# Kernel tuning notes

Hardware: AMD Instinct MI355X
Metric: run time of the kernel (lower is better)

The kernel has to match this reference:

```python
import jax, jax.numpy as jnp
import numpy as np

ALPHA = 0.2   # LeakyReLU negative slope
NEG_INF = -9e15

def setup_inputs() -> dict:
    key = jax.random.key(0)
    k1, k2, k3, k4, k5 = jax.random.split(key, 5)
    B, N, F_IN, F_OUT = 8, 2048, 128, 128
    input = jax.random.normal(k1, (B, N, F_IN), dtype=jnp.float32)
    adj = jax.random.randint(k2, (B, N, N), 0, 2, dtype=jnp.int32)
    W = jax.random.normal(k3, (F_OUT, F_IN), dtype=jnp.float32) * (1.0 / np.sqrt(F_IN))
    a_src = jax.random.normal(k4, (F_OUT, 1), dtype=jnp.float32) * 0.1
    a_dst = jax.random.normal(k5, (F_OUT, 1), dtype=jnp.float32) * 0.1
    return {"input": input, "adj": adj, "W": W, "a_src": a_src, "a_dst": a_dst}

def reference(input, adj, W, a_src, a_dst):
    # h = input @ W^T : [B,N,F_out]
    h = jnp.einsum('bnf,of->bno', input, W)
    src = h @ a_src              # [B,N,1]
    dst = h @ a_dst              # [B,N,1]
    e = src + jnp.swapaxes(dst, 1, 2)          # [B,N,N] additive scores
    e = jnp.where(e > 0, e, ALPHA * e)         # LeakyReLU
    att = jnp.where(adj > 0, e, NEG_INF)
    att = jax.nn.softmax(att, axis=2)
    # dropout is identity in eval mode
    h_prime = jnp.einsum('bnm,bmo->bno', att, h)
    return jax.nn.elu(h_prime)                 # concat=True path
```

## Files before the change

### kernel.cpp

```cpp
#include <hip/hip_runtime.h>
#include <stdint.h>

#define NB 8
#define NN 2048
#define FF 128
#define ALPHA 0.2f

typedef unsigned short u16;
typedef __attribute__((ext_vector_type(8))) short bf16x8;
typedef __attribute__((ext_vector_type(4))) float f32x4;

__device__ __forceinline__ float bf2f(u16 h) {
    union { uint32_t u; float f; } v; v.u = ((uint32_t)h) << 16; return v.f;
}
__device__ __forceinline__ u16 f2bf(float x) {
    union { float f; uint32_t u; } v; v.f = x;
    uint32_t r = v.u + 0x7fffu + ((v.u >> 16) & 1u);
    return (u16)(r >> 16);
}
__device__ __forceinline__ uint4 pack8(const float o[8]) {
    uint4 r;
    r.x = (uint32_t)f2bf(o[0]) | ((uint32_t)f2bf(o[1]) << 16);
    r.y = (uint32_t)f2bf(o[2]) | ((uint32_t)f2bf(o[3]) << 16);
    r.z = (uint32_t)f2bf(o[4]) | ((uint32_t)f2bf(o[5]) << 16);
    r.w = (uint32_t)f2bf(o[6]) | ((uint32_t)f2bf(o[7]) << 16);
    return r;
}
__device__ __forceinline__ void load8f(const float* p, size_t i, float o[8]) {
    float4 a = *(const float4*)(p + i);
    float4 b = *(const float4*)(p + i + 4);
    o[0]=a.x; o[1]=a.y; o[2]=a.z; o[3]=a.w;
    o[4]=b.x; o[5]=b.y; o[6]=b.z; o[7]=b.w;
}

__device__ __forceinline__ void gload_lds16(const void* g, void* l) {
    __builtin_amdgcn_global_load_lds(
        (const __attribute__((address_space(1))) void*)g,
        (__attribute__((address_space(3))) void*)l,
        16, 0, 0);
}

__global__ __launch_bounds__(256) void k_prep(
    const float* __restrict__ x,
    const float* __restrict__ w,
    const float* __restrict__ as_,
    const float* __restrict__ ad_,
    u16* __restrict__ hT,
    float* __restrict__ srcp, float* __restrict__ dstp)
{
    __shared__ __attribute__((aligned(16))) u16 Ws[128][136];
    __shared__ __attribute__((aligned(16))) u16 Xs[64][136];
    __shared__ float waS[128], waD[128];
    __shared__ float lredS[64][4], lredD[64][4];

    const int b  = blockIdx.x & 7;
    const int n0 = (blockIdx.x >> 3) * 64;
    const int t  = threadIdx.x;
    const int wv = t >> 6, lane = t & 63, quad = lane >> 4, lr = lane & 15;

    {
        const int o = t >> 1, fb = (t & 1) * 64;
        #pragma unroll
        for (int k = 0; k < 8; ++k) {
            float v8[8];
            load8f(w, (size_t)o * FF + fb + k * 8, v8);
            *(uint4*)&Ws[o][fb + k * 8] = pack8(v8);
        }
    }
    if (t < 128) {
        float s = 0.f;
        for (int o = 0; o < FF; ++o) s += w[(size_t)o * FF + t] * as_[o];
        waS[t] = s;
    } else {
        const int f = t - 128;
        float s = 0.f;
        for (int o = 0; o < FF; ++o) s += w[(size_t)o * FF + f] * ad_[o];
        waD[f] = s;
    }
    __syncthreads();

    {
        const int r = t >> 2, q = t & 3;
        float sp = 0.f, dp = 0.f;
        #pragma unroll
        for (int k = 0; k < 4; ++k) {
            float v8[8];
            load8f(x, (size_t)(b * NN + n0 + r) * FF + q * 32 + k * 8, v8);
            *(uint4*)&Xs[r][q * 32 + k * 8] = pack8(v8);
            #pragma unroll
            for (int u = 0; u < 8; ++u) {
                sp += v8[u] * waS[q * 32 + k * 8 + u];
                dp += v8[u] * waD[q * 32 + k * 8 + u];
            }
        }
        lredS[r][q] = sp; lredD[r][q] = dp;
    }
    __syncthreads();
    if (t < 64) {
        srcp[b * NN + n0 + t] = lredS[t][0] + lredS[t][1] + lredS[t][2] + lredS[t][3];
        dstp[b * NN + n0 + t] = lredD[t][0] + lredD[t][1] + lredD[t][2] + lredD[t][3];
    }

    f32x4 hacc[8] = {};
    #pragma unroll
    for (int kc = 0; kc < 4; ++kc) {
        const int ko = kc * 32 + quad * 8;
        bf16x8 a = *(const bf16x8*)&Xs[wv * 16 + lr][ko];
        #pragma unroll
        for (int t8 = 0; t8 < 8; ++t8) {
            bf16x8 bb = *(const bf16x8*)&Ws[t8 * 16 + lr][ko];
            hacc[t8] = __builtin_amdgcn_mfma_f32_16x16x32_bf16(a, bb, hacc[t8], 0, 0, 0);
        }
    }
    __syncthreads();

    u16* HsB = &Ws[0][0];
    #pragma unroll
    for (int t8 = 0; t8 < 8; ++t8) {
        #pragma unroll
        for (int reg = 0; reg < 4; ++reg)
            HsB[(t8 * 16 + lr) * 68 + wv * 16 + quad * 4 + reg] = f2bf(hacc[t8][reg]);
    }
    __syncthreads();
    {
        const int r16 = t >> 4, ng = t & 15;
        #pragma unroll
        for (int s = 0; s < 8; ++s) {
            const int o = s * 16 + r16;
            uint2 v = *(const uint2*)&HsB[o * 68 + ng * 4];
            *(uint2*)&hT[(size_t)(b * FF + o) * NN + n0 + ng * 4] = v;
        }
    }
}

__global__ __launch_bounds__(256) void k_attn(
    const int*   __restrict__ adj,
    const u16*   __restrict__ hT,
    const float* __restrict__ srcp,
    const float* __restrict__ dstp,
    float* __restrict__ out)
{
    __shared__ __attribute__((aligned(16))) u16 Hs[128][128];
    __shared__ __attribute__((aligned(16))) u16 Ps[32][136];
    __shared__ float lred[32][8];
    __shared__ float lrowS[32];

    const int b  = blockIdx.x & 7;
    const int i0 = (blockIdx.x >> 3) * 32;
    const int t  = threadIdx.x;
    const int wv = t >> 6, lane = t & 63, quad = lane >> 4, lr = lane & 15;
    const int rowt = (wv & 1) * 16, colt = (wv >> 1) * 64;

    const int il = t >> 3, q = t & 7;
    const float src_i  = srcp[b * NN + i0 + il];
    const int*   adjrow = adj + (size_t)(b * NN + i0 + il) * NN;
    const float* dstb   = dstp + b * NN;

    const int lrow4 = lane >> 4, sl = lane & 15;
    const u16* hTb = hT + (size_t)(b * FF) * NN;
    const int sw = lr & 7;

    f32x4 acc[4] = {};
    float lacc = 0.f;

    for (int j0 = 0; j0 < NN; j0 += 128) {
        #pragma unroll
        for (int i = 0; i < 8; ++i) {
            const int o  = wv * 32 + i * 4 + lrow4;
            const int sg = sl ^ (o & 7);
            gload_lds16(hTb + (size_t)o * NN + j0 + sg * 8, &Hs[wv * 32 + i * 4][0]);
        }
        {
            int4   a4[4]; float4 d4[4];
            #pragma unroll
            for (int it = 0; it < 4; ++it) {
                a4[it] = *(const int4*)(adjrow + j0 + q * 16 + it * 4);
                d4[it] = *(const float4*)(dstb + j0 + q * 16 + it * 4);
            }
            u16 pb[16];
            #pragma unroll
            for (int it = 0; it < 4; ++it) {
                const int*   ai = (const int*)&a4[it];
                const float* dv = (const float*)&d4[it];
                #pragma unroll
                for (int u = 0; u < 4; ++u) {
                    float e = src_i + dv[u];
                    e = e > 0.f ? e : ALPHA * e;
                    float p = __expf(e);
                    p = (ai[u] > 0) ? p : 0.f;
                    const u16 pv = f2bf(p);
                    pb[it * 4 + u] = pv;
                    lacc += bf2f(pv);
                }
            }
            uint4 w0, w1;
            w0.x = (uint32_t)pb[0]  | ((uint32_t)pb[1]  << 16);
            w0.y = (uint32_t)pb[2]  | ((uint32_t)pb[3]  << 16);
            w0.z = (uint32_t)pb[4]  | ((uint32_t)pb[5]  << 16);
            w0.w = (uint32_t)pb[6]  | ((uint32_t)pb[7]  << 16);
            w1.x = (uint32_t)pb[8]  | ((uint32_t)pb[9]  << 16);
            w1.y = (uint32_t)pb[10] | ((uint32_t)pb[11] << 16);
            w1.z = (uint32_t)pb[12] | ((uint32_t)pb[13] << 16);
            w1.w = (uint32_t)pb[14] | ((uint32_t)pb[15] << 16);
            *(uint4*)&Ps[il][q * 16]     = w0;
            *(uint4*)&Ps[il][q * 16 + 8] = w1;
        }
        __syncthreads();

        __builtin_amdgcn_s_setprio(1);
        #pragma unroll
        for (int kc = 0; kc < 4; ++kc) {
            const int ko = kc * 32 + quad * 8;
            bf16x8 a = *(const bf16x8*)&Ps[rowt + lr][ko];
            #pragma unroll
            for (int t8 = 0; t8 < 4; ++t8) {
                bf16x8 bb = *(const bf16x8*)&Hs[colt + t8 * 16 + lr][((kc * 4 + quad) ^ sw) * 8];
                acc[t8] = __builtin_amdgcn_mfma_f32_16x16x32_bf16(a, bb, acc[t8], 0, 0, 0);
            }
        }
        __builtin_amdgcn_s_setprio(0);
        __syncthreads();
    }

    lred[il][q] = lacc;
    __syncthreads();
    if (t < 32) {
        float s = 0.f;
        #pragma unroll
        for (int k = 0; k < 8; ++k) s += lred[t][k];
        lrowS[t] = s;
    }
    __syncthreads();

    #pragma unroll
    for (int t8 = 0; t8 < 4; ++t8) {
        const int col = colt + t8 * 16 + lr;
        #pragma unroll
        for (int reg = 0; reg < 4; ++reg) {
            const int row = rowt + quad * 4 + reg;
            const float l = fmaxf(lrowS[row], 1e-30f);
            float v = acc[t8][reg] / l;
            v = v > 0.f ? v : __expf(v) - 1.f;
            out[(size_t)(b * NN + i0 + row) * FF + col] = v;
        }
    }
}

extern "C" void kernel_launch(void* const* d_in, const int* in_sizes, int n_in,
                              void* d_out, int out_size, void* d_ws, size_t ws_size,
                              hipStream_t stream) {
    const float* x = nullptr; const int* adj = nullptr; const float* w = nullptr;
    const float* as_ = nullptr; const float* ad_ = nullptr;
    for (int i = 0; i < n_in; ++i) {
        const long long s = in_sizes[i];
        if      (s == (long long)NB * NN * FF)  x   = (const float*)d_in[i];
        else if (s == (long long)NB * NN * NN)  adj = (const int*)d_in[i];
        else if (s == FF * FF)                  w   = (const float*)d_in[i];
        else if (s == FF) { if (!as_) as_ = (const float*)d_in[i]; else ad_ = (const float*)d_in[i]; }
    }
    if (!x)   x   = (const float*)d_in[0];
    if (!adj) adj = (const int*)d_in[1];
    if (!w)   w   = (const float*)d_in[2];
    if (!as_) as_ = (const float*)d_in[3];
    if (!ad_) ad_ = (const float*)d_in[4];
    float* out = (float*)d_out;

    u16*   hT   = (u16*)d_ws;
    float* srcp = (float*)((char*)d_ws + (size_t)NB * FF * NN * sizeof(u16));
    float* dstp = srcp + NB * NN;

    k_prep<<<256, 256, 0, stream>>>(x, w, as_, ad_, hT, srcp, dstp);
    k_attn<<<512, 256, 0, stream>>>(adj, hT, srcp, dstp, out);
}
```

Before: 216.5 us.

## Software-pipeline adj/dst register prefetch and Hs staging with manual waitcnt barriers

Restructures the attention loop so that the next tile's adjacency and dst values are loaded into registers through inline-asm global loads while the current tile computes. The next Hs tile is copied into LDS right after the MFMA phase, and `__syncthreads` is replaced by explicit `s_waitcnt` vmcnt/lgkmcnt plus `s_barrier`. It also sets launch bounds to 3 blocks per CU. The aim is to hide global-memory latency on the large int32 adj stream. The cost is higher register pressure and fragile hand-written vmcnt accounting: the copies from the prefetched registers into the current-tile registers could read values before their loads complete.

Result: no change. 215.1 us (-0.7%).

```diff
diff --git a/kernel.cpp b/kernel.cpp
--- a/kernel.cpp
+++ b/kernel.cpp
@@ -9,6 +9,7 @@
 typedef unsigned short u16;
 typedef __attribute__((ext_vector_type(8))) short bf16x8;
 typedef __attribute__((ext_vector_type(4))) float f32x4;
+typedef __attribute__((ext_vector_type(4))) int   i32x4;
 
 __device__ __forceinline__ float bf2f(u16 h) {
     union { uint32_t u; float f; } v; v.u = ((uint32_t)h) << 16; return v.f;
@@ -38,6 +39,25 @@
         (const __attribute__((address_space(1))) void*)g,
         (__attribute__((address_space(3))) void*)l,
         16, 0, 0);
+}
+
+__device__ __forceinline__ void ld4x16_i(const void* p, i32x4& a0, i32x4& a1, i32x4& a2, i32x4& a3) {
+    asm volatile(
+        "global_load_dwordx4 %0, %4, off\n\t"
+        "global_load_dwordx4 %1, %4, off offset:16\n\t"
+        "global_load_dwordx4 %2, %4, off offset:32\n\t"
+        "global_load_dwordx4 %3, %4, off offset:48"
+        : "=&v"(a0), "=&v"(a1), "=&v"(a2), "=&v"(a3)
+        : "v"(p));
+}
+__device__ __forceinline__ void ld4x16_f(const void* p, f32x4& d0, f32x4& d1, f32x4& d2, f32x4& d3) {
+    asm volatile(
+        "global_load_dwordx4 %0, %4, off\n\t"
+        "global_load_dwordx4 %1, %4, off offset:16\n\t"
+        "global_load_dwordx4 %2, %4, off offset:32\n\t"
+        "global_load_dwordx4 %3, %4, off offset:48"
+        : "=&v"(d0), "=&v"(d1), "=&v"(d2), "=&v"(d3)
+        : "v"(p));
 }
 
 __global__ __launch_bounds__(256) void k_prep(
@@ -133,7 +153,7 @@
     }
 }
 
-__global__ __launch_bounds__(256) void k_attn(
+__global__ __launch_bounds__(256, 3) void k_attn(
     const int*   __restrict__ adj,
     const u16*   __restrict__ hT,
     const float* __restrict__ srcp,
@@ -163,36 +183,38 @@
     f32x4 acc[4] = {};
     float lacc = 0.f;
 
-    for (int j0 = 0; j0 < NN; j0 += 128) {
-        #pragma unroll
-        for (int i = 0; i < 8; ++i) {
-            const int o  = wv * 32 + i * 4 + lrow4;
-            const int sg = sl ^ (o & 7);
-            gload_lds16(hTb + (size_t)o * NN + j0 + sg * 8, &Hs[wv * 32 + i * 4][0]);
-        }
+    #define STAGE_HS(J0) { \
+        _Pragma("unroll") for (int i_ = 0; i_ < 8; ++i_) { \
+            const int o_  = wv * 32 + i_ * 4 + lrow4; \
+            const int sg_ = sl ^ (o_ & 7); \
+            gload_lds16(hTb + (size_t)o_ * NN + (J0) + sg_ * 8, &Hs[wv * 32 + i_ * 4][0]); } }
+
+    i32x4 ca0, ca1, ca2, ca3, na0, na1, na2, na3;
+    f32x4 cd0, cd1, cd2, cd3, nd0, nd1, nd2, nd3;
+
+    ld4x16_i(adjrow + q * 16, ca0, ca1, ca2, ca3);
+    ld4x16_f(dstb + q * 16, cd0, cd1, cd2, cd3);
+    STAGE_HS(0);
+
+    const int NT = NN / 128;
+    for (int tt = 0; tt < NT; ++tt) {
+        const int j0 = tt * 128;
+        asm volatile("s_waitcnt vmcnt(8)" ::: "memory");
+        __builtin_amdgcn_sched_barrier(0);
+
         {
-            int4   a4[4]; float4 d4[4];
-            #pragma unroll
-            for (int it = 0; it < 4; ++it) {
-                a4[it] = *(const int4*)(adjrow + j0 + q * 16 + it * 4);
-                d4[it] = *(const float4*)(dstb + j0 + q * 16 + it * 4);
-            }
             u16 pb[16];
-            #pragma unroll
-            for (int it = 0; it < 4; ++it) {
-                const int*   ai = (const int*)&a4[it];
-                const float* dv = (const float*)&d4[it];
-                #pragma unroll
-                for (int u = 0; u < 4; ++u) {
-                    float e = src_i + dv[u];
-                    e = e > 0.f ? e : ALPHA * e;
-                    float p = __expf(e);
-                    p = (ai[u] > 0) ? p : 0.f;
-                    const u16 pv = f2bf(p);
-                    pb[it * 4 + u] = pv;
-                    lacc += bf2f(pv);
-                }
-            }
+            #define PGEN(AV, DV, BASE) { \
+                _Pragma("unroll") for (int u_ = 0; u_ < 4; ++u_) { \
+                    float e_ = src_i + (DV)[u_]; \
+                    e_ = e_ > 0.f ? e_ : ALPHA * e_; \
+                    float p_ = __expf(e_); \
+                    p_ = ((AV)[u_] > 0) ? p_ : 0.f; \
+                    const u16 pv_ = f2bf(p_); \
+                    pb[(BASE) + u_] = pv_; \
+                    lacc += bf2f(pv_); } }
+            PGEN(ca0, cd0, 0) PGEN(ca1, cd1, 4) PGEN(ca2, cd2, 8) PGEN(ca3, cd3, 12)
+            #undef PGEN
             uint4 w0, w1;
             w0.x = (uint32_t)pb[0]  | ((uint32_t)pb[1]  << 16);
             w0.y = (uint32_t)pb[2]  | ((uint32_t)pb[3]  << 16);
@@ -205,7 +227,17 @@
             *(uint4*)&Ps[il][q * 16]     = w0;
             *(uint4*)&Ps[il][q * 16 + 8] = w1;
         }
-        __syncthreads();
+
+        if (tt + 1 < NT) {
+            ld4x16_i(adjrow + j0 + 128 + q * 16, na0, na1, na2, na3);
+            ld4x16_f(dstb + j0 + 128 + q * 16, nd0, nd1, nd2, nd3);
+        }
+
+        if (tt + 1 < NT) asm volatile("s_waitcnt vmcnt(8) lgkmcnt(0)" ::: "memory");
+        else             asm volatile("s_waitcnt vmcnt(0) lgkmcnt(0)" ::: "memory");
+        __builtin_amdgcn_sched_barrier(0);
+        __builtin_amdgcn_s_barrier();
+        __builtin_amdgcn_sched_barrier(0);
 
         __builtin_amdgcn_s_setprio(1);
         #pragma unroll
@@ -219,8 +251,18 @@
             }
         }
         __builtin_amdgcn_s_setprio(0);
-        __syncthreads();
-    }
+
+        asm volatile("s_waitcnt lgkmcnt(0)" ::: "memory");
+        __builtin_amdgcn_sched_barrier(0);
+        __builtin_amdgcn_s_barrier();
+        __builtin_amdgcn_sched_barrier(0);
+
+        if (tt + 1 < NT) STAGE_HS(j0 + 128);
+
+        ca0 = na0; ca1 = na1; ca2 = na2; ca3 = na3;
+        cd0 = nd0; cd1 = nd1; cd2 = nd2; cd3 = nd3;
+    }
+    #undef STAGE_HS
 
     lred[il][q] = lacc;
     __syncthreads();
```
